# Kernel tuning notes

Hardware: AMD Instinct MI355X
Metric: run time of the kernel (lower is better)

## Reference

```python
import jax, jax.numpy as jnp
import numpy as np

B, H, S, DK, DV = 4, 16, 8192, 128, 128

def setup_inputs() -> dict:
    key = jax.random.key(0)
    k1, k2, k3, k4 = jax.random.split(key, 4)
    return {
        "K": jax.random.normal(k1, (B, H, S, DK), dtype=jnp.float32),
        "V": jax.random.normal(k2, (B, H, S, DV), dtype=jnp.float32),
        "M": jax.random.normal(k3, (B, H, DK, DV), dtype=jnp.float32),
        "z": jax.random.uniform(k4, (B, H, DK), dtype=jnp.float32),
    }

def reference(K, V, M, z):
    # phi = ELU(K) + 1  (positive feature map)
    phi_K = jax.nn.elu(K) + 1.0                                   # (B,H,S,dk)
    V_existing = jnp.einsum('bhsk,bhkv->bhsv', phi_K, M)          # (B,H,S,dv)
    delta_M = jnp.einsum('bhsk,bhsv->bhkv', phi_K, V - V_existing)
    new_M = M + delta_M                                           # (B,H,dk,dv)
    new_z = z + phi_K.sum(axis=-2)                                # (B,H,dk)
    return new_M, new_z
```

## Files before the change

### kernel.cpp

```cpp
#include <hip/hip_runtime.h>

#define BH 64
#define SEQ 8192
#define DK 128
#define DV 128
#define NCHUNK 8
#define SC (SEQ / NCHUNK)
#define CS 64
#define NSTAGE (SC / CS)
#define LR 72

typedef _Float16 f16;
typedef _Float16 f16x4 __attribute__((ext_vector_type(4)));
typedef _Float16 f16x8 __attribute__((ext_vector_type(8)));
typedef float f32x4 __attribute__((ext_vector_type(4)));

__global__ __launch_bounds__(256, 2) void delta_phase1(
    const float* __restrict__ Kg, const float* __restrict__ Vg,
    float* __restrict__ newM, float* __restrict__ newZ, float* __restrict__ Gws)
{
  __shared__ f16 phi_lds[DK * LR];
  __shared__ f16 v_lds[DV * LR];

  const int bh    = blockIdx.x >> 3;
  const int chunk = blockIdx.x & 7;
  const int tid   = threadIdx.x;
  const int wave  = tid >> 6;
  const int lane  = tid & 63;
  const int l31   = lane & 31;
  const int lhi   = lane >> 5;
  const int f15_  = lane & 15;
  const int quad  = lane >> 4;

  const float* Kh = Kg + ((size_t)bh * SEQ + (size_t)chunk * SC) * DK;
  const float* Vh = Vg + ((size_t)bh * SEQ + (size_t)chunk * SC) * DV;

  f32x4 acc[8][4];
#pragma unroll
  for (int r = 0; r < 8; ++r)
#pragma unroll
    for (int c = 0; c < 4; ++c)
      acc[r][c] = (f32x4){0.f, 0.f, 0.f, 0.f};

  float zacc[4] = {0.f, 0.f, 0.f, 0.f};

  for (int st = 0; st < NSTAGE; ++st) {
    __syncthreads();
    const float* Ks = Kh + (size_t)st * CS * DK;
    const float* Vs = Vh + (size_t)st * CS * DV;
#pragma unroll
    for (int fj = 0; fj < 4; ++fj) {
      const int feat = fj * 32 + l31;
#pragma unroll
      for (int sq = 0; sq < 2; ++sq) {
        const int srow = wave * 16 + sq * 8 + lhi * 4;
        const float* kp = Ks + (size_t)srow * DK + feat;
        const float a0 = kp[0];
        const float a1 = kp[DK];
        const float a2 = kp[2 * DK];
        const float a3 = kp[3 * DK];
        const float p0 = a0 > 0.f ? a0 + 1.f : __expf(a0);
        const float p1 = a1 > 0.f ? a1 + 1.f : __expf(a1);
        const float p2 = a2 > 0.f ? a2 + 1.f : __expf(a2);
        const float p3 = a3 > 0.f ? a3 + 1.f : __expf(a3);
        zacc[fj] += (p0 + p1) + (p2 + p3);
        *(f16x4*)&phi_lds[feat * LR + srow] =
            (f16x4){(f16)p0, (f16)p1, (f16)p2, (f16)p3};
        const float* vp = Vs + (size_t)srow * DV + feat;
        *(f16x4*)&v_lds[feat * LR + srow] =
            (f16x4){(f16)vp[0], (f16)vp[DV], (f16)vp[2 * DV], (f16)vp[3 * DV]};
      }
    }
    __syncthreads();
#pragma unroll
    for (int ss = 0; ss < 2; ++ss) {
      const int sb = ss * 32 + quad * 8;
      f16x8 bfr[4];
#pragma unroll
      for (int c = 0; c < 4; ++c) {
        const int col = wave * 64 + c * 16;
        const f16* wsrc = (col < DV) ? &v_lds[(col + f15_) * LR]
                                     : &phi_lds[(col - DV + f15_) * LR];
        bfr[c] = *(const f16x8*)&wsrc[sb];
      }
#pragma unroll
      for (int r = 0; r < 8; ++r) {
        const f16x8 afr = *(const f16x8*)&phi_lds[(r * 16 + f15_) * LR + sb];
#pragma unroll
        for (int c = 0; c < 4; ++c)
          acc[r][c] = __builtin_amdgcn_mfma_f32_16x16x32_f16(afr, bfr[c], acc[r][c], 0, 0, 0);
      }
    }
  }

  const size_t mb = (size_t)bh * DK * DV;
#pragma unroll
  for (int r = 0; r < 8; ++r) {
#pragma unroll
    for (int c = 0; c < 4; ++c) {
      const int col = wave * 64 + c * 16 + f15_;
#pragma unroll
      for (int q = 0; q < 4; ++q) {
        const int row = r * 16 + quad * 4 + q;
        const float v = acc[r][c][q];
        if (col < DV)
          atomicAdd(&newM[mb + (size_t)row * DV + col], v);
        else
          atomicAdd(&Gws[mb + (size_t)row * DK + (col - DV)], v);
      }
    }
  }
#pragma unroll
  for (int fj = 0; fj < 4; ++fj) {
    float v = zacc[fj];
    v += __shfl_xor(v, 32, 64);
    if (lhi == 0) atomicAdd(&newZ[bh * DK + fj * 32 + l31], v);
  }
}

__global__ __launch_bounds__(256) void delta_phase2(
    const float* __restrict__ Mg, const float* __restrict__ Gws, float* __restrict__ newM)
{
  __shared__ float Gs[64 * 129];
  __shared__ float Ms[DK * 32];
  const int bh  = blockIdx.x >> 3;
  const int sub = blockIdx.x & 7;
  const int kh  = sub >> 2;
  const int vt  = sub & 3;
  const int tid = threadIdx.x;
  const size_t mb = (size_t)bh * DK * DV;

  for (int i = tid; i < 64 * DK; i += 256)
    Gs[(i >> 7) * 129 + (i & 127)] = Gws[mb + (size_t)(kh * 64 + (i >> 7)) * DK + (i & 127)];
  for (int i = tid; i < DK * 32; i += 256)
    Ms[i] = Mg[mb + (size_t)(i >> 5) * DV + vt * 32 + (i & 31)];
  __syncthreads();

  const int kl = tid >> 2;
  const int vs = (tid & 3) * 8;
  float a[8];
#pragma unroll
  for (int j = 0; j < 8; ++j) a[j] = 0.f;
  for (int kk = 0; kk < DK; ++kk) {
    const float g = Gs[kl * 129 + kk];
#pragma unroll
    for (int j = 0; j < 8; ++j) a[j] += g * Ms[kk * 32 + vs + j];
  }
  float* dst = &newM[mb + (size_t)(kh * 64 + kl) * DV + vt * 32 + vs];
#pragma unroll
  for (int j = 0; j < 8; ++j) dst[j] -= a[j];
}

extern "C" void kernel_launch(void* const* d_in, const int* in_sizes, int n_in,
                              void* d_out, int out_size, void* d_ws, size_t ws_size,
                              hipStream_t stream) {
  const float* Kg = (const float*)d_in[0];
  const float* Vg = (const float*)d_in[1];
  const float* Mg = (const float*)d_in[2];
  const float* zg = (const float*)d_in[3];
  float* out  = (float*)d_out;
  float* newM = out;
  float* newZ = out + (size_t)BH * DK * DV;
  float* Gws  = (float*)d_ws;

  hipMemcpyAsync(newM, Mg, sizeof(float) * (size_t)BH * DK * DV,
                 hipMemcpyDeviceToDevice, stream);
  hipMemcpyAsync(newZ, zg, sizeof(float) * (size_t)BH * DK,
                 hipMemcpyDeviceToDevice, stream);
  hipMemsetAsync(Gws, 0, sizeof(float) * (size_t)BH * DK * DK, stream);

  delta_phase1<<<dim3(BH * NCHUNK), dim3(256), 0, stream>>>(Kg, Vg, newM, newZ, Gws);
  delta_phase2<<<dim3(BH * 8), dim3(256), 0, stream>>>(Mg, Gws, newM);
}
```

Baseline: 592.3 us.

## Split sequence into 16 chunks with 512-thread blocks and deterministic partial reduction

Phase 1 now runs 512-thread blocks, where each wave computes half as many output columns, and uses 16 sequence chunks per head, giving twice as many blocks. Float atomics on M and G are replaced by plain stores of per-chunk partials to workspace, followed by a separate reduce kernel that adds M and removes the memcpy and memset. The aim is more parallelism and occupancy with no atomic contention, at the cost of extra workspace traffic (64 MB of partials) and one extra launch. An atomic fallback path is kept for small workspaces.

```diff
diff --git a/kernel.cpp b/kernel.cpp
--- a/kernel.cpp
+++ b/kernel.cpp
@@ -4,10 +4,7 @@
 #define SEQ 8192
 #define DK 128
 #define DV 128
-#define NCHUNK 8
-#define SC (SEQ / NCHUNK)
 #define CS 64
-#define NSTAGE (SC / CS)
 #define LR 72
 
 typedef _Float16 f16;
@@ -15,15 +12,21 @@
 typedef _Float16 f16x8 __attribute__((ext_vector_type(8)));
 typedef float f32x4 __attribute__((ext_vector_type(4)));
 
-__global__ __launch_bounds__(256, 2) void delta_phase1(
+template <int NC, bool PARTIAL>
+__global__ __launch_bounds__(512, 4) void delta_phase1(
     const float* __restrict__ Kg, const float* __restrict__ Vg,
-    float* __restrict__ newM, float* __restrict__ newZ, float* __restrict__ Gws)
+    float* __restrict__ dstP,
+    float* __restrict__ dstG,
+    float* __restrict__ newZ)
 {
   __shared__ f16 phi_lds[DK * LR];
   __shared__ f16 v_lds[DV * LR];
 
-  const int bh    = blockIdx.x >> 3;
-  const int chunk = blockIdx.x & 7;
+  constexpr int SC  = SEQ / NC;
+  constexpr int NST = SC / CS;
+
+  const int chunk = blockIdx.x;
+  const int bh    = blockIdx.y;
   const int tid   = threadIdx.x;
   const int wave  = tid >> 6;
   const int lane  = tid & 63;
@@ -35,80 +38,88 @@
   const float* Kh = Kg + ((size_t)bh * SEQ + (size_t)chunk * SC) * DK;
   const float* Vh = Vg + ((size_t)bh * SEQ + (size_t)chunk * SC) * DV;
 
-  f32x4 acc[8][4];
+  f32x4 acc[8][2];
 #pragma unroll
   for (int r = 0; r < 8; ++r)
 #pragma unroll
-    for (int c = 0; c < 4; ++c)
+    for (int c = 0; c < 2; ++c)
       acc[r][c] = (f32x4){0.f, 0.f, 0.f, 0.f};
 
   float zacc[4] = {0.f, 0.f, 0.f, 0.f};
 
-  for (int st = 0; st < NSTAGE; ++st) {
+  for (int st = 0; st < NST; ++st) {
     __syncthreads();
     const float* Ks = Kh + (size_t)st * CS * DK;
     const float* Vs = Vh + (size_t)st * CS * DV;
+    const int srow = wave * 8 + lhi * 4;
 #pragma unroll
     for (int fj = 0; fj < 4; ++fj) {
       const int feat = fj * 32 + l31;
-#pragma unroll
-      for (int sq = 0; sq < 2; ++sq) {
-        const int srow = wave * 16 + sq * 8 + lhi * 4;
-        const float* kp = Ks + (size_t)srow * DK + feat;
-        const float a0 = kp[0];
-        const float a1 = kp[DK];
-        const float a2 = kp[2 * DK];
-        const float a3 = kp[3 * DK];
-        const float p0 = a0 > 0.f ? a0 + 1.f : __expf(a0);
-        const float p1 = a1 > 0.f ? a1 + 1.f : __expf(a1);
-        const float p2 = a2 > 0.f ? a2 + 1.f : __expf(a2);
-        const float p3 = a3 > 0.f ? a3 + 1.f : __expf(a3);
-        zacc[fj] += (p0 + p1) + (p2 + p3);
-        *(f16x4*)&phi_lds[feat * LR + srow] =
-            (f16x4){(f16)p0, (f16)p1, (f16)p2, (f16)p3};
-        const float* vp = Vs + (size_t)srow * DV + feat;
-        *(f16x4*)&v_lds[feat * LR + srow] =
-            (f16x4){(f16)vp[0], (f16)vp[DV], (f16)vp[2 * DV], (f16)vp[3 * DV]};
-      }
+      const float* kp = Ks + (size_t)srow * DK + feat;
+      const float a0 = kp[0];
+      const float a1 = kp[DK];
+      const float a2 = kp[2 * DK];
+      const float a3 = kp[3 * DK];
+      const float p0 = a0 > 0.f ? a0 + 1.f : __expf(a0);
+      const float p1 = a1 > 0.f ? a1 + 1.f : __expf(a1);
+      const float p2 = a2 > 0.f ? a2 + 1.f : __expf(a2);
+      const float p3 = a3 > 0.f ? a3 + 1.f : __expf(a3);
+      zacc[fj] += (p0 + p1) + (p2 + p3);
+      *(f16x4*)&phi_lds[feat * LR + srow] =
+          (f16x4){(f16)p0, (f16)p1, (f16)p2, (f16)p3};
+      const float* vp = Vs + (size_t)srow * DV + feat;
+      *(f16x4*)&v_lds[feat * LR + srow] =
+          (f16x4){(f16)vp[0], (f16)vp[DV], (f16)vp[2 * DV], (f16)vp[3 * DV]};
     }
     __syncthreads();
+    const f16* bsrc  = (wave < 4) ? v_lds : phi_lds;
+    const int  cbase = (wave < 4) ? wave * 32 : wave * 32 - 128;
 #pragma unroll
     for (int ss = 0; ss < 2; ++ss) {
       const int sb = ss * 32 + quad * 8;
-      f16x8 bfr[4];
-#pragma unroll
-      for (int c = 0; c < 4; ++c) {
-        const int col = wave * 64 + c * 16;
-        const f16* wsrc = (col < DV) ? &v_lds[(col + f15_) * LR]
-                                     : &phi_lds[(col - DV + f15_) * LR];
-        bfr[c] = *(const f16x8*)&wsrc[sb];
-      }
+      f16x8 bfr[2];
+#pragma unroll
+      for (int c = 0; c < 2; ++c)
+        bfr[c] = *(const f16x8*)&bsrc[(cbase + c * 16 + f15_) * LR + sb];
 #pragma unroll
       for (int r = 0; r < 8; ++r) {
         const f16x8 afr = *(const f16x8*)&phi_lds[(r * 16 + f15_) * LR + sb];
-#pragma unroll
-        for (int c = 0; c < 4; ++c)
-          acc[r][c] = __builtin_amdgcn_mfma_f32_16x16x32_f16(afr, bfr[c], acc[r][c], 0, 0, 0);
+        acc[r][0] = __builtin_amdgcn_mfma_f32_16x16x32_f16(afr, bfr[0], acc[r][0], 0, 0, 0);
+        acc[r][1] = __builtin_amdgcn_mfma_f32_16x16x32_f16(afr, bfr[1], acc[r][1], 0, 0, 0);
       }
     }
   }
 
-  const size_t mb = (size_t)bh * DK * DV;
-#pragma unroll
-  for (int r = 0; r < 8; ++r) {
-#pragma unroll
-    for (int c = 0; c < 4; ++c) {
-      const int col = wave * 64 + c * 16 + f15_;
-#pragma unroll
-      for (int q = 0; q < 4; ++q) {
-        const int row = r * 16 + quad * 4 + q;
-        const float v = acc[r][c][q];
-        if (col < DV)
-          atomicAdd(&newM[mb + (size_t)row * DV + col], v);
-        else
-          atomicAdd(&Gws[mb + (size_t)row * DK + (col - DV)], v);
+  if (PARTIAL) {
+    const size_t pb = (size_t)(bh * NC + chunk) * (128 * 256);
+#pragma unroll
+    for (int r = 0; r < 8; ++r)
+#pragma unroll
+      for (int c = 0; c < 2; ++c) {
+        const int col = wave * 32 + c * 16 + f15_;
+#pragma unroll
+        for (int q = 0; q < 4; ++q) {
+          const int row = r * 16 + quad * 4 + q;
+          dstP[pb + (size_t)row * 256 + col] = acc[r][c][q];
+        }
       }
-    }
+  } else {
+    const size_t mb = (size_t)bh * DK * DV;
+#pragma unroll
+    for (int r = 0; r < 8; ++r)
+#pragma unroll
+      for (int c = 0; c < 2; ++c) {
+        const int col = wave * 32 + c * 16 + f15_;
+#pragma unroll
+        for (int q = 0; q < 4; ++q) {
+          const int row = r * 16 + quad * 4 + q;
+          const float v = acc[r][c][q];
+          if (col < DV)
+            atomicAdd(&dstP[mb + (size_t)row * DV + col], v);
+          else
+            atomicAdd(&dstG[mb + (size_t)row * DK + (col - DV)], v);
+        }
+      }
   }
 #pragma unroll
   for (int fj = 0; fj < 4; ++fj) {
@@ -118,20 +129,57 @@
   }
 }
 
-__global__ __launch_bounds__(256) void delta_phase2(
-    const float* __restrict__ Mg, const float* __restrict__ Gws, float* __restrict__ newM)
+__global__ __launch_bounds__(256) void delta_reduce(
+    const float* __restrict__ Pp, const float* __restrict__ Mg,
+    float* __restrict__ newM, float* __restrict__ Gred, int NC)
+{
+  const int ct  = blockIdx.x;
+  const int bh  = blockIdx.y;
+  const int tid = threadIdx.x;
+  const int col = ct * 32 + (tid & 31);
+  const int r0  = tid >> 5;
+
+  float acc[16];
+#pragma unroll
+  for (int i = 0; i < 16; ++i) acc[i] = 0.f;
+
+  const float* base = Pp + (size_t)(bh * NC) * 32768;
+  for (int ch = 0; ch < NC; ++ch) {
+    const float* p = base + (size_t)ch * 32768;
+#pragma unroll
+    for (int i = 0; i < 16; ++i)
+      acc[i] += p[(size_t)(r0 + 8 * i) * 256 + col];
+  }
+  if (col < 128) {
+#pragma unroll
+    for (int i = 0; i < 16; ++i) {
+      const int row = r0 + 8 * i;
+      newM[(size_t)bh * 16384 + (size_t)row * 128 + col] =
+          Mg[(size_t)bh * 16384 + (size_t)row * 128 + col] + acc[i];
+    }
+  } else {
+#pragma unroll
+    for (int i = 0; i < 16; ++i) {
+      const int row = r0 + 8 * i;
+      Gred[(size_t)bh * 16384 + (size_t)row * 128 + (col - 128)] = acc[i];
+    }
+  }
+}
+
+__global__ __launch_bounds__(256) void delta_gm(
+    const float* __restrict__ Mg, const float* __restrict__ G, float* __restrict__ newM)
 {
   __shared__ float Gs[64 * 129];
   __shared__ float Ms[DK * 32];
-  const int bh  = blockIdx.x >> 3;
-  const int sub = blockIdx.x & 7;
+  const int sub = blockIdx.x;
+  const int bh  = blockIdx.y;
   const int kh  = sub >> 2;
   const int vt  = sub & 3;
   const int tid = threadIdx.x;
   const size_t mb = (size_t)bh * DK * DV;
 
   for (int i = tid; i < 64 * DK; i += 256)
-    Gs[(i >> 7) * 129 + (i & 127)] = Gws[mb + (size_t)(kh * 64 + (i >> 7)) * DK + (i & 127)];
+    Gs[(i >> 7) * 129 + (i & 127)] = G[mb + (size_t)(kh * 64 + (i >> 7)) * DK + (i & 127)];
   for (int i = tid; i < DK * 32; i += 256)
     Ms[i] = Mg[mb + (size_t)(i >> 5) * DV + vt * 32 + (i & 31)];
   __syncthreads();
@@ -161,14 +209,32 @@
   float* out  = (float*)d_out;
   float* newM = out;
   float* newZ = out + (size_t)BH * DK * DV;
-  float* Gws  = (float*)d_ws;
-
-  hipMemcpyAsync(newM, Mg, sizeof(float) * (size_t)BH * DK * DV,
-                 hipMemcpyDeviceToDevice, stream);
+
+  const size_t gredF = (size_t)BH * DK * DK;
+  const size_t need16 = ((size_t)BH * 16 * 32768 + gredF) * sizeof(float);
+  const size_t need8  = ((size_t)BH * 8  * 32768 + gredF) * sizeof(float);
+
   hipMemcpyAsync(newZ, zg, sizeof(float) * (size_t)BH * DK,
                  hipMemcpyDeviceToDevice, stream);
-  hipMemsetAsync(Gws, 0, sizeof(float) * (size_t)BH * DK * DK, stream);
-
-  delta_phase1<<<dim3(BH * NCHUNK), dim3(256), 0, stream>>>(Kg, Vg, newM, newZ, Gws);
-  delta_phase2<<<dim3(BH * 8), dim3(256), 0, stream>>>(Mg, Gws, newM);
-}
+
+  if (ws_size >= need16) {
+    float* Pp   = (float*)d_ws;
+    float* Gred = Pp + (size_t)BH * 16 * 32768;
+    delta_phase1<16, true><<<dim3(16, BH), 512, 0, stream>>>(Kg, Vg, Pp, nullptr, newZ);
+    delta_reduce<<<dim3(8, BH), 256, 0, stream>>>(Pp, Mg, newM, Gred, 16);
+    delta_gm<<<dim3(8, BH), 256, 0, stream>>>(Mg, Gred, newM);
+  } else if (ws_size >= need8) {
+    float* Pp   = (float*)d_ws;
+    float* Gred = Pp + (size_t)BH * 8 * 32768;
+    delta_phase1<8, true><<<dim3(8, BH), 512, 0, stream>>>(Kg, Vg, Pp, nullptr, newZ);
+    delta_reduce<<<dim3(8, BH), 256, 0, stream>>>(Pp, Mg, newM, Gred, 8);
+    delta_gm<<<dim3(8, BH), 256, 0, stream>>>(Mg, Gred, newM);
+  } else {
+    float* Gws = (float*)d_ws;
+    hipMemcpyAsync(newM, Mg, sizeof(float) * (size_t)BH * DK * DV,
+                   hipMemcpyDeviceToDevice, stream);
+    hipMemsetAsync(Gws, 0, sizeof(float) * gredF, stream);
+    delta_phase1<16, false><<<dim3(16, BH), 512, 0, stream>>>(Kg, Vg, newM, Gws, newZ);
+    delta_gm<<<dim3(8, BH), 256, 0, stream>>>(Mg, Gws, newM);
+  }
+}
```

Measured after the change: 587.9 us. About the same (-0.7%).
